# Optimization experiments

Hardware: AMD Instinct MI355X
Metric: run time of the kernel (lower is better)

Reference implementation:

```python
import jax, jax.numpy as jnp
import numpy as np

B, T, E, H, D = 2, 2048, 1024, 16, 64
ROPE_BASE = 10000.0


def project(x, k):
    # Lift to Lorentz hyperboloid with curvature magnitude K=exp(k): <lx,lx>_L = -K
    K = jnp.exp(k)
    x0 = jnp.sqrt(K + jnp.sum(x * x, axis=-1, keepdims=True))
    return jnp.concatenate([x0, x], axis=-1)


def layer_norm(x, w, b, eps=1e-5):
    m = jnp.mean(x, axis=-1, keepdims=True)
    v = jnp.mean((x - m) ** 2, axis=-1, keepdims=True)
    return (x - m) * jax.lax.rsqrt(v + eps) * w + b


def setup_inputs() -> dict:
    key = jax.random.key(0)
    ks = jax.random.split(key, 8)
    s = 0.02
    return dict(
        x=jax.random.normal(ks[0], (B, T, E), jnp.float32),
        block_curvature=jnp.asarray(1.0, jnp.float32),
        mlp_curvature=jnp.asarray(1.0, jnp.float32),
        attn_curvatures=jnp.ones((1, H, 1, 1), jnp.float32),
        w_qkv=jax.random.normal(ks[1], (E + 1, 3 * E), jnp.float32) * s,
        w_attn_proj=jax.random.normal(ks[2], ((D + 1) * H, E), jnp.float32) * s,
        b_attn_proj=jnp.zeros((E,), jnp.float32),
        w_mlp_expand=jax.random.normal(ks[3], (E + 1, 4 * E + 3), jnp.float32) * s,
        b_mlp_expand=jnp.zeros((4 * E + 3,), jnp.float32),
        w_mlp_shrink=jax.random.normal(ks[4], (4 * (E + 1), E), jnp.float32) * s,
        b_mlp_shrink=jnp.zeros((E,), jnp.float32),
        ln_w=jnp.ones((E,), jnp.float32),
        ln_b=jnp.zeros((E,), jnp.float32),
    )


def _block(x, block_curvature, mlp_curvature, attn_curvatures, w_qkv,
           w_attn_proj, b_attn_proj, w_mlp_expand, b_mlp_expand,
           w_mlp_shrink, b_mlp_shrink, ln_w, ln_b):
    Bq, Tq = x.shape[0], x.shape[1]
    lx = project(x, block_curvature)  # (B,T,E+1)

    def block_norm(l):
        return project(layer_norm(l[..., 1:], ln_w, ln_b), block_curvature)

    def skip(l, f):  # hyperbolic skip: add space parts, re-lift
        return project(l[..., 1:] + f[..., 1:], block_curvature)

    def attn(l):
        qkv = l @ w_qkv  # (B,T,3E)
        q, k, v = jnp.split(qkv, 3, axis=-1)
        q = q.reshape(Bq, Tq, H, D)
        k = k.reshape(Bq, Tq, H, D)
        v = v.reshape(Bq, Tq, H, D)
        half = D // 2
        inv_freq = 1.0 / (ROPE_BASE ** (jnp.arange(0, D, 2, dtype=jnp.float32) / D))
        freqs = jnp.arange(Tq, dtype=jnp.float32)[:, None] * inv_freq[None, :]
        cos = jnp.cos(freqs)[None, :, None, :]  # (1,T,1,D/2)
        sin = jnp.sin(freqs)[None, :, None, :]

        def rope(t):
            t1, t2 = t[..., :half], t[..., half:]
            return jnp.concatenate([t1 * cos + t2 * sin, -t1 * sin + t2 * cos], axis=-1)

        q = rope(q).transpose(0, 2, 1, 3)  # (B,H,T,D)
        k = rope(k).transpose(0, 2, 1, 3)
        v = v.transpose(0, 2, 1, 3)
        K = jnp.exp(attn_curvatures)  # (1,H,1,1) per-head curvature
        qt = jnp.sqrt(K + jnp.sum(q * q, axis=-1, keepdims=True))  # time coord (B,H,T,1)
        kt = jnp.sqrt(K + jnp.sum(k * k, axis=-1, keepdims=True))
        lv = project(v, attn_curvatures)  # (B,H,T,D+1)
        # Lorentz inner product without materializing (B,H,T,T,D+1)
        inner = jnp.einsum('bhtd,bhsd->bhts', q, k) - qt * jnp.swapaxes(kt, -1, -2)
        ratio = jnp.maximum(-inner / K, 1.0 + 1e-7)
        dis = jnp.sqrt(K) * jnp.arccosh(ratio)  # (B,H,T,T)
        causal = jnp.tril(jnp.ones((Tq, Tq), dtype=bool))
        w = jnp.where(causal, -dis, -jnp.inf)  # neg_dis attention weight + causal bias
        aw = jax.nn.softmax(w, axis=-1)
        o = jnp.einsum('bhts,bhse->bhte', aw, lv)  # (B,H,T,D+1)
        lnorm2 = o[..., :1] ** 2 - jnp.sum(o[..., 1:] ** 2, axis=-1, keepdims=True)
        hn = jnp.sqrt(jnp.maximum(lnorm2, 1e-12))  # Lorentz norm
        o = o * jnp.sqrt(K) / hn  # renormalize back onto hyperboloid
        o = o.transpose(0, 2, 1, 3).reshape(Bq, Tq, H * (D + 1))
        return project(o @ w_attn_proj + b_attn_proj, block_curvature)

    def mlp(l):
        h = project(l @ w_mlp_expand + b_mlp_expand, mlp_curvature)[..., 1:]  # (B,T,4E+3)
        h = jax.nn.gelu(h, approximate=False)
        h = project(h, mlp_curvature)  # (B,T,4(E+1))
        return project(h @ w_mlp_shrink + b_mlp_shrink, block_curvature)

    lx = skip(lx, attn(block_norm(lx)))
    lx = skip(lx, mlp(block_norm(lx)))
    return lx


def reference(x, block_curvature, mlp_curvature, attn_curvatures, w_qkv,
              w_attn_proj, b_attn_proj, w_mlp_expand, b_mlp_expand,
              w_mlp_shrink, b_mlp_shrink, ln_w, ln_b):
    return _block(x, block_curvature, mlp_curvature, attn_curvatures, w_qkv,
                  w_attn_proj, b_attn_proj, w_mlp_expand, b_mlp_expand,
                  w_mlp_shrink, b_mlp_shrink, ln_w, ln_b)
```

## Files before the change

### kernel.cpp

```cpp
#include <hip/hip_runtime.h>
#include <math.h>

#define MM   4096
#define TT   2048
#define HH   16

typedef __bf16 bf16x8 __attribute__((ext_vector_type(8)));
typedef float f32x4 __attribute__((ext_vector_type(4)));

__device__ __forceinline__ void g2l16(const void* g, void* l) {
    __builtin_amdgcn_global_load_lds(
        (__attribute__((address_space(1))) void*)g,
        (__attribute__((address_space(3))) void*)l, 16, 0, 0);
}

#if __has_builtin(__builtin_amdgcn_exp2f)
__device__ __forceinline__ float fexp2(float x) { return __builtin_amdgcn_exp2f(x); }
#else
__device__ __forceinline__ float fexp2(float x) { return exp2f(x); }
#endif
#if __has_builtin(__builtin_amdgcn_logf)
__device__ __forceinline__ float flog2(float x) { return __builtin_amdgcn_logf(x); }
#else
__device__ __forceinline__ float flog2(float x) { return log2f(x); }
#endif
#if __has_builtin(__builtin_amdgcn_sqrtf)
__device__ __forceinline__ float fsqrt_(float x) { return __builtin_amdgcn_sqrtf(x); }
#else
__device__ __forceinline__ float fsqrt_(float x) { return sqrtf(x); }
#endif
#if __has_builtin(__builtin_amdgcn_rcpf)
__device__ __forceinline__ float frcp_(float x) { return __builtin_amdgcn_rcpf(x); }
#else
__device__ __forceinline__ float frcp_(float x) { return 1.0f / x; }
#endif
#if __has_builtin(__builtin_amdgcn_rsqf)
__device__ __forceinline__ float frsq_(float x) { return __builtin_amdgcn_rsqf(x); }
#else
__device__ __forceinline__ float frsq_(float x) { return rsqrtf(x); }
#endif

__device__ __forceinline__ float gelu_f(float x) {
    float u = 0.7978845608028654f * fmaf(0.044715f * x, x * x, x);
    u = fminf(fmaxf(u, -15.f), 15.f);
    float t = fexp2(-2.885390081777927f * u);
    return 0.5f * x * (1.f + (1.f - t) * frcp_(1.f + t));
}

__device__ __forceinline__ float blockSum256(float v, volatile float* sb) {
    int lane = threadIdx.x & 63, w = threadIdx.x >> 6;
#pragma unroll
    for (int o = 32; o; o >>= 1) v += __shfl_xor(v, o);
    if (lane == 0) sb[w] = v;
    __syncthreads();
    v = sb[0] + sb[1] + sb[2] + sb[3];
    __syncthreads();
    return v;
}

__global__ __launch_bounds__(256) void block_norm_bf_k(
    const float* __restrict__ in, int ld,
    __bf16* __restrict__ out, int ldo,
    const float* __restrict__ lw, const float* __restrict__ lb,
    const float* __restrict__ curv)
{
    int row = blockIdx.x;
    const float* x = in + (size_t)row * ld;
    __bf16* o = out + (size_t)row * ldo;
    __shared__ float sb[4];
    int tid = threadIdx.x;
    float v[4]; float s1 = 0.f, s2 = 0.f;
#pragma unroll
    for (int r = 0; r < 4; r++) {
        float t = x[tid + 256 * r];
        v[r] = t; s1 += t; s2 += t * t;
    }
    s1 = blockSum256(s1, sb);
    s2 = blockSum256(s2, sb);
    float mean = s1 * (1.f / 1024.f);
    float var  = s2 * (1.f / 1024.f) - mean * mean;
    float rs = rsqrtf(var + 1e-5f);
    float y[4]; float ssq = 0.f;
#pragma unroll
    for (int r = 0; r < 4; r++) {
        int i = tid + 256 * r;
        float t = (v[r] - mean) * rs * lw[i] + lb[i];
        y[r] = t; ssq += t * t;
    }
    ssq = blockSum256(ssq, sb);
#pragma unroll
    for (int r = 0; r < 4; r++) o[1 + tid + 256 * r] = (__bf16)y[r];
    if (tid == 0) o[0] = (__bf16)sqrtf(expf(*curv) + ssq);
    if (tid < ldo - 1025) o[1025 + tid] = (__bf16)0.f;
}

__global__ __launch_bounds__(256) void row_x0_k(
    float* __restrict__ buf, int stride, int n, const float* __restrict__ curv)
{
    int row = blockIdx.x;
    float* base = buf + (size_t)row * stride;
    __shared__ float sb[4];
    float s = 0.f;
    for (int i = threadIdx.x; i < n; i += 256) { float t = base[1 + i]; s += t * t; }
    s = blockSum256(s, sb);
    if (threadIdx.x == 0) base[0] = sqrtf(expf(*curv) + s);
}

__global__ __launch_bounds__(256) void row_x0_tail_k(
    __bf16* __restrict__ h,
    const __bf16* __restrict__ ln,
    const __bf16* __restrict__ Bt,
    const float* __restrict__ bias,
    const float* __restrict__ curv)
{
    int row = blockIdx.x;
    __bf16* base = h + (size_t)row * 4224;
    const __bf16* lnr = ln + (size_t)row * 1088;
    const __bf16* B0 = Bt + (size_t)4096 * 1088;
    const __bf16* B1 = Bt + (size_t)4097 * 1088;
    const __bf16* B2 = Bt + (size_t)4098 * 1088;
    __shared__ float sb[4];
    float d0 = 0.f, d1 = 0.f, d2 = 0.f;
    for (int i = threadIdx.x; i < 1088; i += 256) {
        float a = (float)lnr[i];
        d0 += a * (float)B0[i];
        d1 += a * (float)B1[i];
        d2 += a * (float)B2[i];
    }
    d0 = blockSum256(d0, sb);
    d1 = blockSum256(d1, sb);
    d2 = blockSum256(d2, sb);
    float t3[3] = {d0 + bias[4096], d1 + bias[4097], d2 + bias[4098]};
    float ssq_t = 0.f;
#pragma unroll
    for (int j = 0; j < 3; j++) {
        float v = gelu_f(t3[j]);
        t3[j] = v; ssq_t += v * v;
    }
    if (threadIdx.x == 0) {
        base[1 + 4096] = (__bf16)t3[0];
        base[1 + 4097] = (__bf16)t3[1];
        base[1 + 4098] = (__bf16)t3[2];
    }
    float s = 0.f;
    for (int i = threadIdx.x; i < 4096; i += 256) { float t = (float)base[1 + i]; s += t * t; }
    s = blockSum256(s, sb) + ssq_t;
    if (threadIdx.x == 0) base[0] = (__bf16)sqrtf(expf(*curv) + s);
    if (threadIdx.x < 124) base[4100 + threadIdx.x] = (__bf16)0.f;
}

__global__ __launch_bounds__(256) void wt_k(
    const float* __restrict__ W, int K, int N,
    __bf16* __restrict__ Wt, int Kp)
{
    __shared__ float s[32][33];
    int tx = threadIdx.x & 31, ty = threadIdx.x >> 5;
    int k0 = blockIdx.x * 32, n0 = blockIdx.y * 32;
#pragma unroll
    for (int r = 0; r < 4; r++) {
        int k = k0 + ty + 8 * r, n = n0 + tx;
        s[ty + 8 * r][tx] = (k < K && n < N) ? W[(size_t)k * N + n] : 0.f;
    }
    __syncthreads();
#pragma unroll
    for (int r = 0; r < 4; r++) {
        int n = n0 + ty + 8 * r, k = k0 + tx;
        if (n < N) Wt[(size_t)n * Kp + k] = (__bf16)s[tx][ty + 8 * r];
    }
}

template<bool BIAS, bool GELU, bool SKIP, bool OUTBF>
__global__ __launch_bounds__(256, 3) void mgemm128_k(
    const __bf16* __restrict__ A, int lda,
    const __bf16* __restrict__ Bt, int ldb,
    const float* __restrict__ bias,
    const float* __restrict__ skip, int ldskip,
    void* __restrict__ Cout, int ldc,
    int N, int Kp, int nT)
{
    __shared__ __bf16 sAB[24576];
    const int tid = threadIdx.x;
    const int w = tid >> 6, lane = tid & 63;
    const int wm = w >> 1, wn = w & 1;
    const int lr = lane & 15, lq = lane >> 4;

    const int bid = blockIdx.x;
    const int cpx = gridDim.x >> 3;
    const int swz = (bid & 7) * cpx + (bid >> 3);
    const int m0 = (swz / nT) * 128, n0 = (swz % nT) * 128;

    const int rr  = tid >> 2;
    const int csw = ((tid & 3) ^ ((rr >> 1) & 3)) << 3;
    const __bf16* gA[2]; const __bf16* gB[2];
#pragma unroll
    for (int c = 0; c < 2; c++) {
        gA[c] = A + (size_t)(m0 + c * 64 + rr) * lda + csw;
        gB[c] = Bt + (size_t)(n0 + c * 64 + rr) * ldb + csw;
    }
    const int wst = w * 512;

    const int off = (lq ^ ((lr >> 1) & 3)) << 3;
    const int arow = wm * 64 + lr;
    const int brow = wn * 64 + lr;

    f32x4 zero = {0.f, 0.f, 0.f, 0.f};
    f32x4 acc[4][4];
#pragma unroll
    for (int i = 0; i < 4; i++)
#pragma unroll
        for (int j = 0; j < 4; j++) acc[i][j] = zero;

    const int NT = Kp >> 5;
#pragma unroll
    for (int c = 0; c < 2; c++) {
        g2l16(gA[c], sAB + c * 2048 + wst);
        g2l16(gB[c], sAB + 12288 + c * 2048 + wst);
    }
#pragma unroll
    for (int c = 0; c < 2; c++) {
        g2l16(gA[c] + 32, sAB + 4096 + c * 2048 + wst);
        g2l16(gB[c] + 32, sAB + 12288 + 4096 + c * 2048 + wst);
    }
    asm volatile("s_waitcnt vmcnt(4)" ::: "memory");
    __builtin_amdgcn_s_barrier();

    int cur = 0;
    for (int kt = 0; kt < NT; ++kt) {
        if (kt + 2 < NT) {
            const int sbuf = (cur == 0) ? 2 : (cur - 1);
            const int ko = (kt + 2) << 5;
#pragma unroll
            for (int c = 0; c < 2; c++) {
                g2l16(gA[c] + ko, sAB + sbuf * 4096 + c * 2048 + wst);
                g2l16(gB[c] + ko, sAB + 12288 + sbuf * 4096 + c * 2048 + wst);
            }
        }
        const __bf16* pA = sAB + cur * 4096;
        const __bf16* pB = sAB + 12288 + cur * 4096;
        bf16x8 af[4], bf[4];
#pragma unroll
        for (int i = 0; i < 4; i++) af[i] = *(const bf16x8*)&pA[(arow + i * 16) * 32 + off];
#pragma unroll
        for (int j = 0; j < 4; j++) bf[j] = *(const bf16x8*)&pB[(brow + j * 16) * 32 + off];
        __builtin_amdgcn_s_setprio(1);
#pragma unroll
        for (int i = 0; i < 4; i++)
#pragma unroll
            for (int j = 0; j < 4; j++)
                acc[i][j] = __builtin_amdgcn_mfma_f32_16x16x32_bf16(af[i], bf[j], acc[i][j], 0, 0, 0);
        __builtin_amdgcn_s_setprio(0);
        if (kt + 2 < NT) { asm volatile("s_waitcnt vmcnt(4)" ::: "memory"); }
        else             { asm volatile("s_waitcnt vmcnt(0) lgkmcnt(0)" ::: "memory"); }
        __builtin_amdgcn_s_barrier();
        cur = (cur == 2) ? 0 : (cur + 1);
    }

#pragma unroll
    for (int j = 0; j < 4; j++) {
        const int n = n0 + wn * 64 + j * 16 + lr;
        if (n < N) {
            const float bv = BIAS ? bias[n] : 0.f;
#pragma unroll
            for (int i = 0; i < 4; i++) {
#pragma unroll
                for (int r = 0; r < 4; r++) {
                    const int m = m0 + wm * 64 + i * 16 + lq * 4 + r;
                    float v = acc[i][j][r] + bv;
                    if (GELU) v = gelu_f(v);
                    if (SKIP) v += skip[(size_t)m * ldskip + n];
                    if (OUTBF) ((__bf16*)Cout)[(size_t)m * ldc + n] = (__bf16)v;
                    else       ((float*)Cout)[(size_t)m * ldc + n] = v;
                }
            }
        }
    }
}

__global__ __launch_bounds__(256) void rope_k(
    float* __restrict__ QKV, const float* __restrict__ curv,
    float* __restrict__ qt, float* __restrict__ kt,
    __bf16* __restrict__ Kb, __bf16* __restrict__ Obf)
{
    int row = blockIdx.x;
    int b = row >> 11, t = row & (TT - 1);
    int wv = threadIdx.x >> 6, d = threadIdx.x & 63;
    int j = d & 31;
    float fr = (float)t * powf(10000.0f, -(float)(2 * j) / 64.0f);
    float cv = cosf(fr), sv = sinf(fr);
    float sgn = (d < 32) ? sv : -sv;
    for (int h = wv; h < HH; h += 4) {
        float Kh = expf(curv[h]);
        float* base = QKV + (size_t)row * 3072 + h * 64;
        float q = base[d], k = base[1024 + d];
        float qp = __shfl_xor(q, 32);
        float kp = __shfl_xor(k, 32);
        float qr = q * cv + qp * sgn;
        float kr = k * cv + kp * sgn;
        base[d] = qr;
        size_t oidx = ((size_t)(b * HH + h) * TT + t);
        Kb[oidx * 64 + d] = (__bf16)kr;
        float sq = qr * qr, sk = kr * kr;
#pragma unroll
        for (int o = 32; o; o >>= 1) {
            sq += __shfl_xor(sq, o);
            sk += __shfl_xor(sk, o);
        }
        if (d == 0) {
            qt[oidx] = sqrtf(Kh + sq);
            kt[oidx] = sqrtf(Kh + sk);
        }
    }
    if (threadIdx.x < 48) Obf[(size_t)row * 1088 + 1040 + threadIdx.x] = (__bf16)0.f;
}

__global__ __launch_bounds__(256) void vtrans_k(
    const float* __restrict__ QKV, const float* __restrict__ curv,
    __bf16* __restrict__ Vtb, float* __restrict__ vt)
{
    __shared__ float sT[64 * 65];
    int bh = blockIdx.y; int h = bh & (HH - 1); int b = bh >> 4;
    int t0 = blockIdx.x * 64;
    int tid = threadIdx.x, w = tid >> 6, lane = tid & 63;
    float Kh = expf(curv[h]);
    const float* vbase = QKV + (size_t)(b * TT + t0) * 3072 + 2048 + h * 64;
#pragma unroll 4
    for (int i = 0; i < 16; i++) {
        int tr = w * 16 + i;
        float v = vbase[(size_t)tr * 3072 + lane];
        sT[lane * 65 + tr] = v;
        float s = v * v;
#pragma unroll
        for (int o = 32; o; o >>= 1) s += __shfl_xor(s, o);
        if (lane == 0) vt[(size_t)bh * TT + t0 + tr] = sqrtf(Kh + s);
    }
    __syncthreads();
    int d = tid >> 2, seg = tid & 3;
    const float* r = &sT[d * 65 + seg * 16];
    bf16x8 o0, o1;
#pragma unroll
    for (int i = 0; i < 8; i++) { o0[i] = (__bf16)r[i]; o1[i] = (__bf16)r[8 + i]; }
    __bf16* dst = Vtb + ((size_t)bh * 64 + d) * TT + t0 + seg * 16;
    *(bf16x8*)dst = o0;
    *(bf16x8*)(dst + 8) = o1;
}

__global__ __launch_bounds__(256, 3) void flash_k(
    const float* __restrict__ QKV,
    const __bf16* __restrict__ Kb, const __bf16* __restrict__ Vtb,
    const float* __restrict__ qt, const float* __restrict__ kt,
    const float* __restrict__ vt,
    const float* __restrict__ curv,
    __bf16* __restrict__ O)
{
    __shared__ __bf16 sK[2][4096];
    __shared__ __bf16 sVt[2][4096];
    __shared__ __bf16 sP[4 * 16 * 72];
    __shared__ float skt[2][64], svt[2][64];

    int bh = blockIdx.x; int h = bh & (HH - 1); int b = bh >> 4;
    int qti = 31 - (int)blockIdx.y;
    int q0 = qti << 6;
    int NJ = qti + 1;
    float Kh = expf(curv[h]);
    float sqKh = sqrtf(Kh), msqK = -sqKh, invKh = 1.0f / Kh;
    const float* tok = QKV + (size_t)b * TT * 3072 + h * 64;
    const char* KbB = (const char*)Kb + (size_t)bh * TT * 128;
    const char* VtB = (const char*)Vtb + (size_t)bh * 64 * (TT * 2);
    const float* qtp = qt + (size_t)bh * TT;
    const float* ktp = kt + (size_t)bh * TT;
    const float* vtp = vt + (size_t)bh * TT;

    int tid = threadIdx.x;
    int w = tid >> 6, lane = tid & 63;
    int m = lane & 15, quad = lane >> 4;
    int myBase = q0 + 16 * w;
    __bf16* sPw = &sP[w * 16 * 72];

    bf16x8 qhi[2], qlo[2];
    {
        const float* qrow = tok + (size_t)(myBase + m) * 3072;
#pragma unroll
        for (int ks = 0; ks < 2; ks++) {
            const float* s = qrow + quad * 8 + 32 * ks;
            float4 f0 = *(const float4*)s;
            float4 f1 = *(const float4*)(s + 4);
            float fa[8] = {f0.x, f0.y, f0.z, f0.w, f1.x, f1.y, f1.z, f1.w};
#pragma unroll
            for (int jj = 0; jj < 8; jj++) {
                __bf16 hv = (__bf16)fa[jj];
                qhi[ks][jj] = hv;
                qlo[ks][jj] = (__bf16)(fa[jj] - (float)hv);
            }
        }
    }
    float qtv[4]; int qg[4];
#pragma unroll
    for (int r = 0; r < 4; r++) { qg[r] = myBase + quad * 4 + r; qtv[r] = qtp[qg[r]]; }

    f32x4 zero = {0.f, 0.f, 0.f, 0.f};
    f32x4 accO[4];
#pragma unroll
    for (int nt = 0; nt < 4; nt++) accO[nt] = zero;
    float lsumr[4] = {}, o0r[4] = {};

    {
        const char* kg = KbB + (size_t)lane * 128 + w * 16;
        char* sKb = (char*)&sK[0][0] + w * 1024;
        g2l16(kg,      sKb);
        g2l16(kg + 64, sKb + 4096);
        const char* vg = VtB + (size_t)lane * (TT * 2) + w * 16;
        char* sVb = (char*)&sVt[0][0] + w * 1024;
        g2l16(vg,      sVb);
        g2l16(vg + 64, sVb + 4096);
    }
    if (tid < 64) skt[0][tid] = ktp[tid];
    else if (tid < 128) svt[0][tid - 64] = vtp[tid - 64];
    __syncthreads();

    for (int j = 0; j < NJ; ++j) {
        int cur = j & 1;
        int sb = j << 6;
        if (j + 1 < NJ) {
            int sb2 = sb + 64;
            const char* kg = KbB + (size_t)(sb2 + lane) * 128 + w * 16;
            char* sKb = (char*)&sK[cur ^ 1][0] + w * 1024;
            g2l16(kg,      sKb);
            g2l16(kg + 64, sKb + 4096);
            const char* vg = VtB + (size_t)lane * (TT * 2) + sb2 * 2 + w * 16;
            char* sVb = (char*)&sVt[cur ^ 1][0] + w * 1024;
            g2l16(vg,      sVb);
            g2l16(vg + 64, sVb + 4096);
            if (tid < 64) skt[cur ^ 1][tid] = ktp[sb2 + tid];
            else if (tid < 128) svt[cur ^ 1][tid - 64] = vtp[sb2 + tid - 64];
        }

        f32x4 accS[4];
#pragma unroll
        for (int nt = 0; nt < 4; nt++) accS[nt] = zero;
#pragma unroll
        for (int nt = 0; nt < 4; nt++) {
#pragma unroll
            for (int ksp = 0; ksp < 2; ksp++) {
                bf16x8 bk = *(const bf16x8*)&sK[cur][((ksp * 4 + quad) * 64 + nt * 16 + m) * 8];
                accS[nt] = __builtin_amdgcn_mfma_f32_16x16x32_bf16(qhi[ksp], bk, accS[nt], 0, 0, 0);
                accS[nt] = __builtin_amdgcn_mfma_f32_16x16x32_bf16(qlo[ksp], bk, accS[nt], 0, 0, 0);
            }
        }
#pragma unroll
        for (int nt = 0; nt < 4; nt++) {
            int col = nt * 16 + m;
            int sglob = sb + col;
            float ktv = skt[cur][col], vtv = svt[cur][col];
#pragma unroll
            for (int r = 0; r < 4; r++) {
                float dot = accS[nt][r];
                float rdiff = fmaf(qtv[r], ktv, -dot);
                float ratio = fmaxf(rdiff * invKh, 1.0f + 1e-7f);
                float y = ratio + fsqrt_(fmaf(ratio, ratio, -1.0f));
                float pv = fexp2(msqK * flog2(y));
                float p = (sglob <= qg[r]) ? pv : 0.0f;
                lsumr[r] += p;
                o0r[r] = fmaf(p, vtv, o0r[r]);
                sPw[(quad * 4 + r) * 72 + col] = (__bf16)p;
            }
        }
        __asm__ volatile("s_waitcnt lgkmcnt(0)" ::: "memory");
#pragma unroll
        for (int ksp = 0; ksp < 2; ksp++) {
            bf16x8 aP = *(const bf16x8*)&sPw[m * 72 + ksp * 32 + quad * 8];
#pragma unroll
            for (int nt = 0; nt < 4; nt++) {
                bf16x8 bV = *(const bf16x8*)&sVt[cur][((ksp * 4 + quad) * 64 + nt * 16 + m) * 8];
                accO[nt] = __builtin_amdgcn_mfma_f32_16x16x32_bf16(aP, bV, accO[nt], 0, 0, 0);
            }
        }
        __syncthreads();
    }

#pragma unroll
    for (int r = 0; r < 4; r++) {
#pragma unroll
        for (int off = 1; off < 16; off <<= 1) {
            lsumr[r] += __shfl_xor(lsumr[r], off);
            o0r[r]   += __shfl_xor(o0r[r], off);
        }
    }
#pragma unroll
    for (int r = 0; r < 4; r++) {
        float inv = frcp_(lsumr[r]);
        float o0f = o0r[r] * inv;
        float ov[4]; float part = 0.f;
#pragma unroll
        for (int nt = 0; nt < 4; nt++) { float t = accO[nt][r] * inv; ov[nt] = t; part += t * t; }
        part += __shfl_xor(part, 1);
        part += __shfl_xor(part, 2);
        part += __shfl_xor(part, 4);
        part += __shfl_xor(part, 8);
        float scale = sqKh * frsq_(fmaxf(o0f * o0f - part, 1e-12f));
        size_t orow = (size_t)(b * TT + qg[r]) * 1088 + h * 65;
        if (m == 0) O[orow] = (__bf16)(o0f * scale);
#pragma unroll
        for (int nt = 0; nt < 4; nt++) O[orow + 1 + nt * 16 + m] = (__bf16)(ov[nt] * scale);
    }
}

extern "C" void kernel_launch(void* const* d_in, const int* in_sizes, int n_in,
                              void* d_out, int out_size, void* d_ws, size_t ws_size,
                              hipStream_t stream) {
    const float* x    = (const float*)d_in[0];
    const float* bc   = (const float*)d_in[1];
    const float* mc   = (const float*)d_in[2];
    const float* ac   = (const float*)d_in[3];
    const float* w_qkv = (const float*)d_in[4];
    const float* w_ap  = (const float*)d_in[5];
    const float* b_ap  = (const float*)d_in[6];
    const float* w_me  = (const float*)d_in[7];
    const float* b_me  = (const float*)d_in[8];
    const float* w_ms  = (const float*)d_in[9];
    const float* b_ms  = (const float*)d_in[10];
    const float* lnw  = (const float*)d_in[11];
    const float* lnb  = (const float*)d_in[12];
    float* out = (float*)d_out;
    float* ws  = (float*)d_ws;

    float* R      = ws;
    float* qkvbuf = R;
    float* X2     = R;
    __bf16* h_bf  = (__bf16*)(R + 4194304);
    float* p      = R + 12845056;
    __bf16* ln_bf = (__bf16*)p;  p += 2228224;
    __bf16* o_bf  = (__bf16*)p;  p += 2228224;
    __bf16* qkvT  = (__bf16*)p;  p += 1671168;
    __bf16* apT   = (__bf16*)p;  p += 557056;
    float*  meT_f = p;           p += 2229856;
    float*  msT_f = p;           p += 2162688;
    float* Qt = p;               p += 2 * HH * TT;
    float* Kt = p;               p += 2 * HH * TT;
    float* Vt = p;
    __bf16* meT = (__bf16*)meT_f;
    __bf16* msT = (__bf16*)msT_f;
    __bf16* Kb  = (__bf16*)meT_f;
    __bf16* Vtb = (__bf16*)msT_f;

    wt_k<<<dim3(34, 96),  256, 0, stream>>>(w_qkv, 1025, 3072, qkvT, 1088);
    wt_k<<<dim3(34, 32),  256, 0, stream>>>(w_ap,  1040, 1024, apT,  1088);

    block_norm_bf_k<<<MM, 256, 0, stream>>>(x, 1024, ln_bf, 1088, lnw, lnb, bc);
    mgemm128_k<false, false, false, false><<<dim3(768), 256, 0, stream>>>(
        ln_bf, 1088, qkvT, 1088, nullptr, nullptr, 0, qkvbuf, 3072, 3072, 1088, 24);
    rope_k<<<MM, 256, 0, stream>>>(qkvbuf, ac, Qt, Kt, Kb, o_bf);
    vtrans_k<<<dim3(32, 32), 256, 0, stream>>>(qkvbuf, ac, Vtb, Vt);
    flash_k<<<dim3(2 * HH, 32), 256, 0, stream>>>(qkvbuf, Kb, Vtb, Qt, Kt, Vt, ac, o_bf);
    wt_k<<<dim3(34, 129), 256, 0, stream>>>(w_me,  1025, 4099, meT, 1088);
    wt_k<<<dim3(132, 32), 256, 0, stream>>>(w_ms,  4100, 1024, msT, 4224);
    mgemm128_k<true, false, true, false><<<dim3(256), 256, 0, stream>>>(
        o_bf, 1088, apT, 1088, b_ap, x, 1024, X2, 1024, 1024, 1088, 8);
    block_norm_bf_k<<<MM, 256, 0, stream>>>(X2, 1024, ln_bf, 1088, lnw, lnb, bc);
    mgemm128_k<true, true, false, true><<<dim3(1024), 256, 0, stream>>>(
        ln_bf, 1088, meT, 1088, b_me, nullptr, 0, (void*)(h_bf + 1), 4224, 4096, 1088, 32);
    row_x0_tail_k<<<MM, 256, 0, stream>>>(h_bf, ln_bf, meT, b_me, mc);
    mgemm128_k<true, false, true, false><<<dim3(256), 256, 0, stream>>>(
        h_bf, 4224, msT, 4224, b_ms, X2, 1024, (void*)(out + 1), 1025, 1024, 4224, 8);
    row_x0_k<<<MM, 256, 0, stream>>>(out, 1025, 1024, bc);
}
```

Baseline: 457.4 us.

## Realign GEMM outputs, rotate shrink weights, and regroup tile swizzle per XCD

The MLP hidden buffer now stores its x0 coordinate at the end of the row instead of the front, and the shrink weight transpose rotates its K index to match. This lets the expand GEMM write to an aligned base rather than an offset-by-one address. The shrink GEMM now writes to an aligned 1024-stride scratch buffer. A new final kernel copies that into the 1025-stride output and computes x0, in place of the old in-place x0 kernel. The GEMM block swizzle also assigns each XCD a compact 2D region of M×N tiles to improve L2 reuse. The cost is an extra copy pass over the output.

```diff
diff --git a/kernel.cpp b/kernel.cpp
--- a/kernel.cpp
+++ b/kernel.cpp
@@ -94,16 +94,22 @@
     if (tid < ldo - 1025) o[1025 + tid] = (__bf16)0.f;
 }
 
-__global__ __launch_bounds__(256) void row_x0_k(
-    float* __restrict__ buf, int stride, int n, const float* __restrict__ curv)
+__global__ __launch_bounds__(256) void out_final_k(
+    float* __restrict__ out, const float* __restrict__ P,
+    const float* __restrict__ curv)
 {
     int row = blockIdx.x;
-    float* base = buf + (size_t)row * stride;
+    const float* p = P + (size_t)row * 1024;
+    float* o = out + (size_t)row * 1025;
     __shared__ float sb[4];
-    float s = 0.f;
-    for (int i = threadIdx.x; i < n; i += 256) { float t = base[1 + i]; s += t * t; }
+    int tid = threadIdx.x;
+    float v[4]; float s = 0.f;
+#pragma unroll
+    for (int r = 0; r < 4; r++) { float t = p[tid + 256 * r]; v[r] = t; s += t * t; }
     s = blockSum256(s, sb);
-    if (threadIdx.x == 0) base[0] = sqrtf(expf(*curv) + s);
+#pragma unroll
+    for (int r = 0; r < 4; r++) o[1 + tid + 256 * r] = v[r];
+    if (tid == 0) o[0] = sqrtf(expf(*curv) + s);
 }
 
 __global__ __launch_bounds__(256) void row_x0_tail_k(
@@ -138,17 +144,18 @@
         t3[j] = v; ssq_t += v * v;
     }
     if (threadIdx.x == 0) {
-        base[1 + 4096] = (__bf16)t3[0];
-        base[1 + 4097] = (__bf16)t3[1];
-        base[1 + 4098] = (__bf16)t3[2];
+        base[4096] = (__bf16)t3[0];
+        base[4097] = (__bf16)t3[1];
+        base[4098] = (__bf16)t3[2];
     }
     float s = 0.f;
-    for (int i = threadIdx.x; i < 4096; i += 256) { float t = (float)base[1 + i]; s += t * t; }
+    for (int i = threadIdx.x; i < 4096; i += 256) { float t = (float)base[i]; s += t * t; }
     s = blockSum256(s, sb) + ssq_t;
-    if (threadIdx.x == 0) base[0] = (__bf16)sqrtf(expf(*curv) + s);
+    if (threadIdx.x == 0) base[4099] = (__bf16)sqrtf(expf(*curv) + s);
     if (threadIdx.x < 124) base[4100 + threadIdx.x] = (__bf16)0.f;
 }
 
+template<bool ROT>
 __global__ __launch_bounds__(256) void wt_k(
     const float* __restrict__ W, int K, int N,
     __bf16* __restrict__ Wt, int Kp)
@@ -165,7 +172,8 @@
 #pragma unroll
     for (int r = 0; r < 4; r++) {
         int n = n0 + ty + 8 * r, k = k0 + tx;
-        if (n < N) Wt[(size_t)n * Kp + k] = (__bf16)s[tx][ty + 8 * r];
+        int kd = (ROT && k < K) ? ((k == 0) ? (K - 1) : (k - 1)) : k;
+        if (n < N) Wt[(size_t)n * Kp + kd] = (__bf16)s[tx][ty + 8 * r];
     }
 }
 
@@ -185,9 +193,12 @@
     const int lr = lane & 15, lq = lane >> 4;
 
     const int bid = blockIdx.x;
-    const int cpx = gridDim.x >> 3;
-    const int swz = (bid & 7) * cpx + (bid >> 3);
-    const int m0 = (swz / nT) * 128, n0 = (swz % nT) * 128;
+    const int xcd = bid & 7, loc = bid >> 3;
+    const int nH = nT >> 1;
+    const int mH = (gridDim.x >> 3) / nH;
+    const int mt = (xcd >> 1) * mH + loc / nH;
+    const int nt = (xcd & 1) * nH + loc % nH;
+    const int m0 = mt * 128, n0 = nt * 128;
 
     const int rr  = tid >> 2;
     const int csw = ((tid & 3) ^ ((rr >> 1) & 3)) << 3;
@@ -541,9 +552,10 @@
     __bf16* msT = (__bf16*)msT_f;
     __bf16* Kb  = (__bf16*)meT_f;
     __bf16* Vtb = (__bf16*)msT_f;
-
-    wt_k<<<dim3(34, 96),  256, 0, stream>>>(w_qkv, 1025, 3072, qkvT, 1088);
-    wt_k<<<dim3(34, 32),  256, 0, stream>>>(w_ap,  1040, 1024, apT,  1088);
+    float* Pbuf = (float*)ln_bf;
+
+    wt_k<false><<<dim3(34, 96),  256, 0, stream>>>(w_qkv, 1025, 3072, qkvT, 1088);
+    wt_k<false><<<dim3(34, 32),  256, 0, stream>>>(w_ap,  1040, 1024, apT,  1088);
 
     block_norm_bf_k<<<MM, 256, 0, stream>>>(x, 1024, ln_bf, 1088, lnw, lnb, bc);
     mgemm128_k<false, false, false, false><<<dim3(768), 256, 0, stream>>>(
@@ -551,15 +563,15 @@
     rope_k<<<MM, 256, 0, stream>>>(qkvbuf, ac, Qt, Kt, Kb, o_bf);
     vtrans_k<<<dim3(32, 32), 256, 0, stream>>>(qkvbuf, ac, Vtb, Vt);
     flash_k<<<dim3(2 * HH, 32), 256, 0, stream>>>(qkvbuf, Kb, Vtb, Qt, Kt, Vt, ac, o_bf);
-    wt_k<<<dim3(34, 129), 256, 0, stream>>>(w_me,  1025, 4099, meT, 1088);
-    wt_k<<<dim3(132, 32), 256, 0, stream>>>(w_ms,  4100, 1024, msT, 4224);
+    wt_k<false><<<dim3(34, 129), 256, 0, stream>>>(w_me,  1025, 4099, meT, 1088);
+    wt_k<true ><<<dim3(132, 32), 256, 0, stream>>>(w_ms,  4100, 1024, msT, 4224);
     mgemm128_k<true, false, true, false><<<dim3(256), 256, 0, stream>>>(
         o_bf, 1088, apT, 1088, b_ap, x, 1024, X2, 1024, 1024, 1088, 8);
     block_norm_bf_k<<<MM, 256, 0, stream>>>(X2, 1024, ln_bf, 1088, lnw, lnb, bc);
     mgemm128_k<true, true, false, true><<<dim3(1024), 256, 0, stream>>>(
-        ln_bf, 1088, meT, 1088, b_me, nullptr, 0, (void*)(h_bf + 1), 4224, 4096, 1088, 32);
+        ln_bf, 1088, meT, 1088, b_me, nullptr, 0, (void*)h_bf, 4224, 4096, 1088, 32);
     row_x0_tail_k<<<MM, 256, 0, stream>>>(h_bf, ln_bf, meT, b_me, mc);
     mgemm128_k<true, false, true, false><<<dim3(256), 256, 0, stream>>>(
-        h_bf, 4224, msT, 4224, b_ms, X2, 1024, (void*)(out + 1), 1025, 1024, 4224, 8);
-    row_x0_k<<<MM, 256, 0, stream>>>(out, 1025, 1024, bc);
-}
+        h_bf, 4224, msT, 4224, b_ms, X2, 1024, (void*)Pbuf, 1024, 1024, 4224, 8);
+    out_final_k<<<MM, 256, 0, stream>>>(out, Pbuf, bc);
+}
```

Result: faster. 447.7 us (-2.1%).
